# Kernel optimization log

Measured on AMD Instinct MI355X. Metric: run time of the kernel, lower is better.

## Reference

```python
import jax, jax.numpy as jnp
import numpy as np

N = 50000      # nodes
E = 600000     # edges
G = 512        # graphs in batch
F_IN = 128     # input node features
H = 128        # hidden size (both layers)
PH = 128       # pool/classifier hidden size


def setup_inputs() -> dict:
    key = jax.random.key(0)
    ks = jax.random.split(key, 12)
    def lin(k, fi, fo):
        return (jax.random.normal(k, (fi, fo), jnp.float32) / np.sqrt(fi)).astype(jnp.float32)
    return {
        "x": jax.random.normal(ks[0], (N, F_IN), jnp.float32),
        "edge_index": jax.random.randint(ks[1], (2, E), 0, N),
        "batch": jnp.sort(jax.random.randint(ks[2], (N,), 0, G)),
        "W1": lin(ks[3], F_IN, H), "b1": jnp.zeros((H,), jnp.float32),
        "ln1_g": jnp.ones((H,), jnp.float32), "ln1_b": jnp.zeros((H,), jnp.float32),
        "W2": lin(ks[4], H, H), "b2": jnp.zeros((H,), jnp.float32),
        "ln2_g": jnp.ones((H,), jnp.float32), "ln2_b": jnp.zeros((H,), jnp.float32),
        "gate_w1": lin(ks[5], H, PH), "gate_b1": jnp.zeros((PH,), jnp.float32),
        "gate_w2": lin(ks[6], PH, 1), "gate_b2": jnp.zeros((1,), jnp.float32),
        "cls_w1": lin(ks[7], H, PH), "cls_b1": jnp.zeros((PH,), jnp.float32),
        "cls_w2": lin(ks[8], PH, 2), "cls_b2": jnp.zeros((2,), jnp.float32),
    }


def _layer_norm(h, g, b):
    m = h.mean(-1, keepdims=True)
    v = ((h - m) ** 2).mean(-1, keepdims=True)
    return (h - m) * jax.lax.rsqrt(v + 1e-5) * g + b


def _gcn(x, src, dst, norm, W, b):
    # GCNConv: x' = D^{-1/2} (A+I) D^{-1/2} (x W) + b
    h = x @ W
    out = jax.ops.segment_sum(h[src] * norm[:, None], dst, num_segments=N)
    return out + b


def reference(x, edge_index, batch, W1, b1, ln1_g, ln1_b, W2, b2, ln2_g, ln2_b,
              gate_w1, gate_b1, gate_w2, gate_b2, cls_w1, cls_b1, cls_w2, cls_b2):
    loops = jnp.arange(N, dtype=edge_index.dtype)
    src = jnp.concatenate([edge_index[0], loops])
    dst = jnp.concatenate([edge_index[1], loops])
    deg = jax.ops.segment_sum(jnp.ones_like(src, dtype=x.dtype), dst, num_segments=N)
    dinv = jnp.where(deg > 0, jax.lax.rsqrt(jnp.maximum(deg, 1e-12)), 0.0)
    norm = dinv[src] * dinv[dst]  # [(E+N)]

    h = jax.nn.relu(_layer_norm(_gcn(x, src, dst, norm, W1, b1), ln1_g, ln1_b))
    h = jax.nn.relu(_layer_norm(_gcn(h, src, dst, norm, W2, b2), ln2_g, ln2_b))

    # GlobalAttention pooling: gate MLP -> scatter softmax over graphs -> weighted sum
    gate = (jax.nn.relu(h @ gate_w1 + gate_b1) @ gate_w2 + gate_b2)[:, 0]  # [N]
    gmax = jax.ops.segment_max(gate, batch, num_segments=G)
    a = jnp.exp(gate - gmax[batch])
    denom = jax.ops.segment_sum(a, batch, num_segments=G)
    alpha = a / denom[batch]
    pooled = jax.ops.segment_sum(alpha[:, None] * h, batch, num_segments=G)  # [G, H]

    logits = jax.nn.relu(pooled @ cls_w1 + cls_b1) @ cls_w2 + cls_b2  # [G, 2]
    return logits
```

## Files before the change

kernel.cpp:

```cpp
#include <hip/hip_runtime.h>
#include <hip/hip_bf16.h>

typedef short s8v __attribute__((ext_vector_type(8)));
typedef float f4v __attribute__((ext_vector_type(4)));

#define LDA 136

__device__ __forceinline__ unsigned short f2bf(float f) {
  unsigned int u = __builtin_bit_cast(unsigned int, f);
  unsigned int r = u + 0x7fffu + ((u >> 16) & 1u);
  return (unsigned short)(r >> 16);
}
__device__ __forceinline__ float bf2f(unsigned short s) {
  return __builtin_bit_cast(float, ((unsigned int)s) << 16);
}
__device__ __forceinline__ float bflo(unsigned int v) {
  return __builtin_bit_cast(float, (unsigned int)(v << 16));
}
__device__ __forceinline__ float bfhi(unsigned int v) {
  return __builtin_bit_cast(float, (unsigned int)(v & 0xffff0000u));
}
__device__ __forceinline__ unsigned int packbf(float a, float b) {
  return (unsigned int)f2bf(a) | ((unsigned int)f2bf(b) << 16);
}

__device__ __forceinline__ int lower_bound_i(const int* a, int n, int key) {
  int lo = 0, hi = n;
  while (lo < hi) { int mid = (lo + hi) >> 1; if (a[mid] < key) lo = mid + 1; else hi = mid; }
  return lo;
}

__device__ __forceinline__ void gather_node(
    int i, int sub, const int* __restrict__ offs, const int2* __restrict__ col2,
    const float* __restrict__ dinv, const uint4* __restrict__ hu,
    const float* __restrict__ bias, float v[8]) {
  float di = dinv[i];
  float sl = di * di;
  uint4 hv = hu[(size_t)i * 16 + sub];
  float4 b0v = reinterpret_cast<const float4*>(bias)[sub * 2];
  float4 b1v = reinterpret_cast<const float4*>(bias)[sub * 2 + 1];
  v[0] = bflo(hv.x) * sl + b0v.x; v[1] = bfhi(hv.x) * sl + b0v.y;
  v[2] = bflo(hv.y) * sl + b0v.z; v[3] = bfhi(hv.y) * sl + b0v.w;
  v[4] = bflo(hv.z) * sl + b1v.x; v[5] = bfhi(hv.z) * sl + b1v.y;
  v[6] = bflo(hv.w) * sl + b1v.z; v[7] = bfhi(hv.w) * sl + b1v.w;
  int b0 = offs[i], b1 = offs[i + 1];
  int e = b0;
  for (; e + 4 <= b1; e += 4) {
    int2 c0 = col2[e], c1 = col2[e + 1], c2 = col2[e + 2], c3 = col2[e + 3];
    uint4 h0 = hu[(size_t)c0.x * 16 + sub];
    uint4 h1 = hu[(size_t)c1.x * 16 + sub];
    uint4 h2 = hu[(size_t)c2.x * 16 + sub];
    uint4 h3 = hu[(size_t)c3.x * 16 + sub];
    float n0 = __builtin_bit_cast(float, c0.y) * di;
    float n1 = __builtin_bit_cast(float, c1.y) * di;
    float n2 = __builtin_bit_cast(float, c2.y) * di;
    float n3 = __builtin_bit_cast(float, c3.y) * di;
    v[0] += bflo(h0.x) * n0 + bflo(h1.x) * n1 + bflo(h2.x) * n2 + bflo(h3.x) * n3;
    v[1] += bfhi(h0.x) * n0 + bfhi(h1.x) * n1 + bfhi(h2.x) * n2 + bfhi(h3.x) * n3;
    v[2] += bflo(h0.y) * n0 + bflo(h1.y) * n1 + bflo(h2.y) * n2 + bflo(h3.y) * n3;
    v[3] += bfhi(h0.y) * n0 + bfhi(h1.y) * n1 + bfhi(h2.y) * n2 + bfhi(h3.y) * n3;
    v[4] += bflo(h0.z) * n0 + bflo(h1.z) * n1 + bflo(h2.z) * n2 + bflo(h3.z) * n3;
    v[5] += bfhi(h0.z) * n0 + bfhi(h1.z) * n1 + bfhi(h2.z) * n2 + bfhi(h3.z) * n3;
    v[6] += bflo(h0.w) * n0 + bflo(h1.w) * n1 + bflo(h2.w) * n2 + bflo(h3.w) * n3;
    v[7] += bfhi(h0.w) * n0 + bfhi(h1.w) * n1 + bfhi(h2.w) * n2 + bfhi(h3.w) * n3;
  }
  for (; e < b1; ++e) {
    int2 c0 = col2[e];
    uint4 h0 = hu[(size_t)c0.x * 16 + sub];
    float n0 = __builtin_bit_cast(float, c0.y) * di;
    v[0] += bflo(h0.x) * n0; v[1] += bfhi(h0.x) * n0;
    v[2] += bflo(h0.y) * n0; v[3] += bfhi(h0.y) * n0;
    v[4] += bflo(h0.z) * n0; v[5] += bfhi(h0.z) * n0;
    v[6] += bflo(h0.w) * n0; v[7] += bfhi(h0.w) * n0;
  }
}

__device__ __forceinline__ uint4 ln_relu_pack(
    float v[8], int sub, const float* __restrict__ gam, const float* __restrict__ bet) {
  float s = 0.f, q = 0.f;
#pragma unroll
  for (int j = 0; j < 8; ++j) { s += v[j]; q += v[j] * v[j]; }
#pragma unroll
  for (int o = 1; o < 16; o <<= 1) {
    s += __shfl_xor(s, o);
    q += __shfl_xor(q, o);
  }
  float m = s * (1.0f / 128.0f);
  float var = q * (1.0f / 128.0f) - m * m;
  float rs = rsqrtf(var + 1e-5f);
  float4 g0 = reinterpret_cast<const float4*>(gam)[sub * 2];
  float4 g1 = reinterpret_cast<const float4*>(gam)[sub * 2 + 1];
  float4 e0 = reinterpret_cast<const float4*>(bet)[sub * 2];
  float4 e1 = reinterpret_cast<const float4*>(bet)[sub * 2 + 1];
  uint4 ov;
  ov.x = packbf(fmaxf((v[0] - m) * rs * g0.x + e0.x, 0.f), fmaxf((v[1] - m) * rs * g0.y + e0.y, 0.f));
  ov.y = packbf(fmaxf((v[2] - m) * rs * g0.z + e0.z, 0.f), fmaxf((v[3] - m) * rs * g0.w + e0.w, 0.f));
  ov.z = packbf(fmaxf((v[4] - m) * rs * g1.x + e1.x, 0.f), fmaxf((v[5] - m) * rs * g1.y + e1.y, 0.f));
  ov.w = packbf(fmaxf((v[6] - m) * rs * g1.z + e1.z, 0.f), fmaxf((v[7] - m) * rs * g1.w + e1.w, 0.f));
  return ov;
}

__global__ __launch_bounds__(256) void pack_zero(
    const float* __restrict__ Wa, const float* __restrict__ Wb, const float* __restrict__ Wc,
    unsigned short* __restrict__ P, unsigned int* __restrict__ deg, int n) {
  int bid = blockIdx.x;
  if (bid >= 384) {
    int i = (bid - 384) * 256 + threadIdx.x;
    if (i < n) deg[i] = 0u;
    return;
  }
  int gidx = bid * 256 + threadIdx.x;
  int which = gidx >> 15;
  int idx = gidx & 32767;
  const float* W = (which == 0) ? Wa : (which == 1) ? Wb : Wc;
  int j = idx & 15;
  int lane = (idx >> 4) & 63;
  int t = (idx >> 10) & 7;
  int c = (idx >> 13) & 3;
  int k = c * 32 + (lane >> 4) * 8 + (j & 7);
  int nn = t * 16 + (lane & 15);
  float f = W[k * 128 + nn];
  unsigned short hi = f2bf(f);
  unsigned short outv = (j < 8) ? hi : f2bf(f - bf2f(hi));
  P[gidx] = outv;
}

__global__ void accum_deg(const int* __restrict__ dst, unsigned int* __restrict__ deg, int E) {
  int e = blockIdx.x * blockDim.x + threadIdx.x;
  if (e < E) atomicAdd(&deg[dst[e]], 1u);
}

__global__ __launch_bounds__(256) void scanA(const unsigned int* __restrict__ deg,
                                             int* __restrict__ offs, int* __restrict__ partial,
                                             float* __restrict__ dinv, int n) {
  __shared__ int sh[256];
  int t = threadIdx.x;
  int i = blockIdx.x * 256 + t;
  int v = (i < n) ? (int)deg[i] : 0;
  if (i < n) dinv[i] = rsqrtf((float)(deg[i] + 1u));
  sh[t] = v;
  __syncthreads();
  for (int o = 1; o < 256; o <<= 1) {
    int add = (t >= o) ? sh[t - o] : 0;
    __syncthreads();
    sh[t] += add;
    __syncthreads();
  }
  if (i < n) offs[i] = sh[t] - v;
  if (t == 255) partial[blockIdx.x] = sh[255];
}

__global__ __launch_bounds__(256) void scanC(int* __restrict__ offs, const int* __restrict__ partial,
                                             int* __restrict__ cursor, int n, int E) {
  __shared__ int red[256];
  int bid = blockIdx.x;
  int t = threadIdx.x;
  int s = 0;
  for (int j = t; j < bid; j += 256) s += partial[j];
  red[t] = s;
  __syncthreads();
#pragma unroll
  for (int o = 128; o > 0; o >>= 1) {
    if (t < o) red[t] += red[t + o];
    __syncthreads();
  }
  int pre = red[0];
  int i = bid * 256 + t;
  if (i < n) {
    int o = offs[i] + pre;
    offs[i] = o;
    cursor[i] = o;
  }
  if (i == 0) offs[n] = E;
}

__global__ __launch_bounds__(256) void gemm1_scatter(
    const float* __restrict__ in, const unsigned short* __restrict__ P,
    unsigned short* __restrict__ out, int n,
    const int* __restrict__ src, const int* __restrict__ dst,
    int* __restrict__ cursor, int2* __restrict__ col2,
    const float* __restrict__ dinv, int E, int gemmBlocks) {
  if ((int)blockIdx.x >= gemmBlocks) {
    int e = ((int)blockIdx.x - gemmBlocks) * 256 + threadIdx.x;
    if (e < E) {
      int d = dst[e];
      int s = src[e];
      int slot = atomicAdd(&cursor[d], 1);
      col2[slot] = make_int2(s, __builtin_bit_cast(int, dinv[s]));
    }
    return;
  }
  int tid = threadIdx.x;
  int wave = tid >> 6, lane = tid & 63;
  int quad = lane >> 4, col = lane & 15;
  int base = blockIdx.x * 64 + wave * 16;
  int m = base + col;

  f4v acc[8];
#pragma unroll
  for (int t = 0; t < 8; ++t) acc[t] = (f4v){0.f, 0.f, 0.f, 0.f};

  for (int c = 0; c < 4; ++c) {
    s8v ah, al;
    float v[8];
    if (m < n) {
      const float4* xp = reinterpret_cast<const float4*>(in + (size_t)m * 128 + c * 32 + quad * 8);
      float4 v0 = xp[0], v1 = xp[1];
      v[0] = v0.x; v[1] = v0.y; v[2] = v0.z; v[3] = v0.w;
      v[4] = v1.x; v[5] = v1.y; v[6] = v1.z; v[7] = v1.w;
    } else {
#pragma unroll
      for (int j = 0; j < 8; ++j) v[j] = 0.f;
    }
#pragma unroll
    for (int j = 0; j < 8; ++j) {
      unsigned short h = f2bf(v[j]);
      ah[j] = (short)h;
      al[j] = (short)f2bf(v[j] - bf2f(h));
    }
#pragma unroll
    for (int t = 0; t < 8; ++t) {
      const s8v* bp = reinterpret_cast<const s8v*>(&P[((c * 8 + t) * 64 + lane) * 16]);
      s8v bh = bp[0], bl = bp[1];
      acc[t] = __builtin_amdgcn_mfma_f32_16x16x32_bf16(ah, bh, acc[t], 0, 0, 0);
      acc[t] = __builtin_amdgcn_mfma_f32_16x16x32_bf16(ah, bl, acc[t], 0, 0, 0);
      acc[t] = __builtin_amdgcn_mfma_f32_16x16x32_bf16(al, bh, acc[t], 0, 0, 0);
    }
  }
#pragma unroll
  for (int t = 0; t < 8; ++t)
#pragma unroll
    for (int r = 0; r < 4; ++r) {
      int mm = base + quad * 4 + r;
      if (mm < n) out[(size_t)mm * 128 + t * 16 + col] = f2bf(acc[t][r]);
    }
}

__global__ __launch_bounds__(256) void gather_gemm(
    const int* __restrict__ offs, const int2* __restrict__ col2,
    const float* __restrict__ dinv, const unsigned short* __restrict__ h,
    const float* __restrict__ bias, const float* __restrict__ gam,
    const float* __restrict__ bet, const unsigned short* __restrict__ P,
    unsigned short* __restrict__ out, int n) {
  __shared__ unsigned short A[64 * LDA];
  int tid = threadIdx.x;
  int wave = tid >> 6, lane = tid & 63;
  int grp = lane >> 4, sub = lane & 15;
  const uint4* hu = reinterpret_cast<const uint4*>(h);
  int blk = blockIdx.x * 64;
  for (int it = 0; it < 4; ++it) {
    int li = it * 16 + wave * 4 + grp;
    int i = blk + li;
    uint4 ov;
    if (i < n) {
      float v[8];
      gather_node(i, sub, offs, col2, dinv, hu, bias, v);
      ov = ln_relu_pack(v, sub, gam, bet);
    } else {
      ov = make_uint4(0u, 0u, 0u, 0u);
    }
    *reinterpret_cast<uint4*>(&A[li * LDA + sub * 8]) = ov;
  }
  __syncthreads();
  int quad = lane >> 4, col = lane & 15;
  f4v acc[8];
#pragma unroll
  for (int t = 0; t < 8; ++t) acc[t] = (f4v){0.f, 0.f, 0.f, 0.f};
  int liA = wave * 16 + col;
  for (int c = 0; c < 4; ++c) {
    s8v ah = *reinterpret_cast<const s8v*>(&A[liA * LDA + c * 32 + quad * 8]);
#pragma unroll
    for (int t = 0; t < 8; ++t) {
      const s8v* bp = reinterpret_cast<const s8v*>(&P[((c * 8 + t) * 64 + lane) * 16]);
      s8v bh = bp[0], bl = bp[1];
      acc[t] = __builtin_amdgcn_mfma_f32_16x16x32_bf16(ah, bh, acc[t], 0, 0, 0);
      acc[t] = __builtin_amdgcn_mfma_f32_16x16x32_bf16(ah, bl, acc[t], 0, 0, 0);
    }
  }
#pragma unroll
  for (int t = 0; t < 8; ++t)
#pragma unroll
    for (int r = 0; r < 4; ++r) {
      int mm = blk + wave * 16 + quad * 4 + r;
      if (mm < n) out[(size_t)mm * 128 + t * 16 + col] = f2bf(acc[t][r]);
    }
}

__global__ __launch_bounds__(256) void gather_gate(
    const int* __restrict__ offs, const int2* __restrict__ col2,
    const float* __restrict__ dinv, const unsigned short* __restrict__ h,
    const float* __restrict__ bias, const float* __restrict__ gam,
    const float* __restrict__ bet, const unsigned short* __restrict__ P,
    const float* __restrict__ gb1, const float* __restrict__ gw2,
    const float* __restrict__ gb2, unsigned short* __restrict__ hout,
    float* __restrict__ gate, int n) {
  __shared__ unsigned short A[64 * LDA];
  int tid = threadIdx.x;
  int wave = tid >> 6, lane = tid & 63;
  int grp = lane >> 4, sub = lane & 15;
  const uint4* hu = reinterpret_cast<const uint4*>(h);
  int blk = blockIdx.x * 64;
  for (int it = 0; it < 4; ++it) {
    int li = it * 16 + wave * 4 + grp;
    int i = blk + li;
    uint4 ov;
    if (i < n) {
      float v[8];
      gather_node(i, sub, offs, col2, dinv, hu, bias, v);
      ov = ln_relu_pack(v, sub, gam, bet);
      reinterpret_cast<uint4*>(hout)[(size_t)i * 16 + sub] = ov;
    } else {
      ov = make_uint4(0u, 0u, 0u, 0u);
    }
    *reinterpret_cast<uint4*>(&A[li * LDA + sub * 8]) = ov;
  }
  __syncthreads();
  int quad = lane >> 4, col = lane & 15;
  f4v acc[8];
#pragma unroll
  for (int t = 0; t < 8; ++t) acc[t] = (f4v){0.f, 0.f, 0.f, 0.f};
  int liA = wave * 16 + col;
  for (int c = 0; c < 4; ++c) {
    s8v ah = *reinterpret_cast<const s8v*>(&A[liA * LDA + c * 32 + quad * 8]);
#pragma unroll
    for (int t = 0; t < 8; ++t) {
      const s8v* bp = reinterpret_cast<const s8v*>(&P[((c * 8 + t) * 64 + lane) * 16]);
      s8v bh = bp[0], bl = bp[1];
      acc[t] = __builtin_amdgcn_mfma_f32_16x16x32_bf16(ah, bh, acc[t], 0, 0, 0);
      acc[t] = __builtin_amdgcn_mfma_f32_16x16x32_bf16(ah, bl, acc[t], 0, 0, 0);
    }
  }
  float bv[8], g2[8];
#pragma unroll
  for (int t = 0; t < 8; ++t) {
    bv[t] = gb1[t * 16 + col];
    g2[t] = gw2[t * 16 + col];
  }
  float gb2v = gb2[0];
#pragma unroll
  for (int r = 0; r < 4; ++r) {
    float p = 0.f;
#pragma unroll
    for (int t = 0; t < 8; ++t)
      p += fmaxf(acc[t][r] + bv[t], 0.f) * g2[t];
#pragma unroll
    for (int o = 1; o < 16; o <<= 1) p += __shfl_xor(p, o);
    int mm = blk + wave * 16 + quad * 4 + r;
    if (col == 0 && mm < n) gate[mm] = p + gb2v;
  }
}

__global__ __launch_bounds__(256) void pool_cls(
    float* __restrict__ gate, const unsigned short* __restrict__ h,
    const int* __restrict__ batch,
    const float* __restrict__ w1, const float* __restrict__ b1,
    const float* __restrict__ w2, const float* __restrict__ b2,
    float* __restrict__ out, int n) {
  int g = blockIdx.x;
  int tid = threadIdx.x;
  __shared__ float red[256];
  __shared__ float red2[256];
  __shared__ float p[128];
  __shared__ float r[128];
  int lo = lower_bound_i(batch, n, g);
  int hi = lower_bound_i(batch, n, g + 1);
  if (lo >= hi) {
    if (tid < 128) p[tid] = 0.0f;
  } else {
    float m = -3.0e38f;
    for (int i = lo + tid; i < hi; i += 256) m = fmaxf(m, gate[i]);
    red[tid] = m;
    __syncthreads();
#pragma unroll
    for (int o = 128; o > 0; o >>= 1) {
      if (tid < o) red[tid] = fmaxf(red[tid], red[tid + o]);
      __syncthreads();
    }
    m = red[0];
    __syncthreads();
    float s = 0.0f;
    for (int i = lo + tid; i < hi; i += 256) {
      float e = __expf(gate[i] - m);
      gate[i] = e;
      s += e;
    }
    red[tid] = s;
    __syncthreads();
#pragma unroll
    for (int o = 128; o > 0; o >>= 1) {
      if (tid < o) red[tid] += red[tid + o];
      __syncthreads();
    }
    float inv = 1.0f / red[0];
    __syncthreads();
    const unsigned int* hu = reinterpret_cast<const unsigned int*>(h);
    int j = tid & 63, rgp = tid >> 6;
    float a0 = 0.f, a1 = 0.f;
    int i = lo + rgp;
    for (; i + 4 < hi; i += 8) {
      unsigned int p0 = hu[(size_t)i * 64 + j];
      unsigned int p1 = hu[(size_t)(i + 4) * 64 + j];
      float w0 = gate[i], w1v = gate[i + 4];
      a0 += bflo(p0) * w0 + bflo(p1) * w1v;
      a1 += bfhi(p0) * w0 + bfhi(p1) * w1v;
    }
    if (i < hi) {
      unsigned int p0 = hu[(size_t)i * 64 + j];
      float w0 = gate[i];
      a0 += bflo(p0) * w0;
      a1 += bfhi(p0) * w0;
    }
    red[tid] = a0;
    red2[tid] = a1;
    __syncthreads();
    if (tid < 64) {
      p[2 * tid]     = (red[tid] + red[tid + 64] + red[tid + 128] + red[tid + 192]) * inv;
      p[2 * tid + 1] = (red2[tid] + red2[tid + 64] + red2[tid + 128] + red2[tid + 192]) * inv;
    }
  }
  __syncthreads();
  int j = tid & 127, half = tid >> 7;
  float acc = 0.0f;
#pragma unroll 8
  for (int k = half * 64; k < half * 64 + 64; ++k)
    acc = fmaf(p[k], w1[k * 128 + j], acc);
  red[tid] = acc;
  __syncthreads();
  if (tid < 128) r[tid] = fmaxf(red[tid] + red[tid + 128] + b1[tid], 0.0f);
  __syncthreads();
  if (tid < 2) {
    float a = 0.0f;
    for (int k = 0; k < 128; ++k) a = fmaf(r[k], w2[k * 2 + tid], a);
    out[g * 2 + tid] = a + b2[tid];
  }
}

static inline size_t alup(size_t x) { return (x + 255) & ~(size_t)255; }

extern "C" void kernel_launch(void* const* d_in, const int* in_sizes, int n_in,
                              void* d_out, int out_size, void* d_ws, size_t ws_size,
                              hipStream_t stream) {
  const float* x    = (const float*)d_in[0];
  const int*   ei   = (const int*)d_in[1];
  const int*   bat  = (const int*)d_in[2];
  const float* W1   = (const float*)d_in[3];
  const float* b1   = (const float*)d_in[4];
  const float* ln1g = (const float*)d_in[5];
  const float* ln1b = (const float*)d_in[6];
  const float* W2   = (const float*)d_in[7];
  const float* b2   = (const float*)d_in[8];
  const float* ln2g = (const float*)d_in[9];
  const float* ln2b = (const float*)d_in[10];
  const float* gw1  = (const float*)d_in[11];
  const float* gb1  = (const float*)d_in[12];
  const float* gw2  = (const float*)d_in[13];
  const float* gb2  = (const float*)d_in[14];
  const float* cw1  = (const float*)d_in[15];
  const float* cb1  = (const float*)d_in[16];
  const float* cw2  = (const float*)d_in[17];
  const float* cb2  = (const float*)d_in[18];

  const int N = in_sizes[2];
  const int E = in_sizes[1] / 2;
  const int G = out_size / 2;
  const int* src = ei;
  const int* dst = ei + E;

  int nb256 = (N + 255) / 256;
  int eb256 = (E + 255) / 256;
  int mfmaB = (N + 63) / 64;

  char* base = (char*)d_ws;
  unsigned int* deg = (unsigned int*)base; base += alup((size_t)N * 4);
  float* dinv = (float*)base;              base += alup((size_t)N * 4);
  int* offs = (int*)base;                  base += alup((size_t)(N + 1) * 4);
  int* cursor = (int*)base;                base += alup((size_t)N * 4);
  int* partial = (int*)base;               base += alup((size_t)nb256 * 4);
  int2* col2 = (int2*)base;                base += alup((size_t)E * 8);
  unsigned short* pW = (unsigned short*)base; base += alup((size_t)3 * 32768 * 2);
  unsigned short* hbuf = (unsigned short*)base;  base += alup((size_t)N * 128 * 2);
  unsigned short* hbuf2 = (unsigned short*)base; base += alup((size_t)N * 128 * 2);
  unsigned short* hout = (unsigned short*)base;  base += alup((size_t)N * 128 * 2);
  float* gate = (float*)base;              base += alup((size_t)N * 4);

  unsigned short* pW1 = pW;
  unsigned short* pW2 = pW + 32768;
  unsigned short* pG1 = pW + 65536;

  float* out = (float*)d_out;

  pack_zero<<<384 + nb256, 256, 0, stream>>>(W1, W2, gw1, pW, deg, N);
  accum_deg<<<eb256, 256, 0, stream>>>(dst, deg, E);
  scanA<<<nb256, 256, 0, stream>>>(deg, offs, partial, dinv, N);
  scanC<<<nb256, 256, 0, stream>>>(offs, partial, cursor, N, E);
  gemm1_scatter<<<mfmaB + eb256, 256, 0, stream>>>(x, pW1, hbuf, N,
                                                   src, dst, cursor, col2, dinv, E, mfmaB);
  gather_gemm<<<mfmaB, 256, 0, stream>>>(offs, col2, dinv, hbuf, b1, ln1g, ln1b,
                                         pW2, hbuf2, N);
  gather_gate<<<mfmaB, 256, 0, stream>>>(offs, col2, dinv, hbuf2, b2, ln2g, ln2b,
                                         pG1, gb1, gw2, gb2, hout, gate, N);
  pool_cls<<<G, 256, 0, stream>>>(gate, hout, bat, cw1, cb1, cw2, cb2, out, N);
}
```

Baseline: 266.0 us.

## Fold source-side degree normalization into GEMM epilogue and shrink CSR to indices

The GEMM epilogues now pre-scale each output row by dinv of that node, so the gather only sums neighbor rows and multiplies once by the destination dinv. This lets the CSR array hold plain int source indices instead of (index, dinv) pairs, halving edge-array traffic and removing the per-edge dinv load during scatter and the per-edge multiplies in the gather. It adds a rounding step, because the pre-scaled values are stored in bf16.

After: 272.3 us. +2.4%, slower.

```diff
diff --git a/kernel.cpp b/kernel.cpp
--- a/kernel.cpp
+++ b/kernel.cpp
@@ -30,48 +30,38 @@
   return lo;
 }
 
-__device__ __forceinline__ void gather_node(
-    int i, int sub, const int* __restrict__ offs, const int2* __restrict__ col2,
-    const float* __restrict__ dinv, const uint4* __restrict__ hu,
-    const float* __restrict__ bias, float v[8]) {
-  float di = dinv[i];
-  float sl = di * di;
+__device__ __forceinline__ void gather_sum(
+    int i, int sub, const int* __restrict__ offs, const int* __restrict__ col,
+    const uint4* __restrict__ hu, float acc[8]) {
   uint4 hv = hu[(size_t)i * 16 + sub];
-  float4 b0v = reinterpret_cast<const float4*>(bias)[sub * 2];
-  float4 b1v = reinterpret_cast<const float4*>(bias)[sub * 2 + 1];
-  v[0] = bflo(hv.x) * sl + b0v.x; v[1] = bfhi(hv.x) * sl + b0v.y;
-  v[2] = bflo(hv.y) * sl + b0v.z; v[3] = bfhi(hv.y) * sl + b0v.w;
-  v[4] = bflo(hv.z) * sl + b1v.x; v[5] = bfhi(hv.z) * sl + b1v.y;
-  v[6] = bflo(hv.w) * sl + b1v.z; v[7] = bfhi(hv.w) * sl + b1v.w;
+  acc[0] = bflo(hv.x); acc[1] = bfhi(hv.x);
+  acc[2] = bflo(hv.y); acc[3] = bfhi(hv.y);
+  acc[4] = bflo(hv.z); acc[5] = bfhi(hv.z);
+  acc[6] = bflo(hv.w); acc[7] = bfhi(hv.w);
   int b0 = offs[i], b1 = offs[i + 1];
   int e = b0;
   for (; e + 4 <= b1; e += 4) {
-    int2 c0 = col2[e], c1 = col2[e + 1], c2 = col2[e + 2], c3 = col2[e + 3];
-    uint4 h0 = hu[(size_t)c0.x * 16 + sub];
-    uint4 h1 = hu[(size_t)c1.x * 16 + sub];
-    uint4 h2 = hu[(size_t)c2.x * 16 + sub];
-    uint4 h3 = hu[(size_t)c3.x * 16 + sub];
-    float n0 = __builtin_bit_cast(float, c0.y) * di;
-    float n1 = __builtin_bit_cast(float, c1.y) * di;
-    float n2 = __builtin_bit_cast(float, c2.y) * di;
-    float n3 = __builtin_bit_cast(float, c3.y) * di;
-    v[0] += bflo(h0.x) * n0 + bflo(h1.x) * n1 + bflo(h2.x) * n2 + bflo(h3.x) * n3;
-    v[1] += bfhi(h0.x) * n0 + bfhi(h1.x) * n1 + bfhi(h2.x) * n2 + bfhi(h3.x) * n3;
-    v[2] += bflo(h0.y) * n0 + bflo(h1.y) * n1 + bflo(h2.y) * n2 + bflo(h3.y) * n3;
-    v[3] += bfhi(h0.y) * n0 + bfhi(h1.y) * n1 + bfhi(h2.y) * n2 + bfhi(h3.y) * n3;
-    v[4] += bflo(h0.z) * n0 + bflo(h1.z) * n1 + bflo(h2.z) * n2 + bflo(h3.z) * n3;
-    v[5] += bfhi(h0.z) * n0 + bfhi(h1.z) * n1 + bfhi(h2.z) * n2 + bfhi(h3.z) * n3;
-    v[6] += bflo(h0.w) * n0 + bflo(h1.w) * n1 + bflo(h2.w) * n2 + bflo(h3.w) * n3;
-    v[7] += bfhi(h0.w) * n0 + bfhi(h1.w) * n1 + bfhi(h2.w) * n2 + bfhi(h3.w) * n3;
+    int s0 = col[e], s1 = col[e + 1], s2 = col[e + 2], s3 = col[e + 3];
+    uint4 h0 = hu[(size_t)s0 * 16 + sub];
+    uint4 h1 = hu[(size_t)s1 * 16 + sub];
+    uint4 h2 = hu[(size_t)s2 * 16 + sub];
+    uint4 h3 = hu[(size_t)s3 * 16 + sub];
+    acc[0] += bflo(h0.x) + bflo(h1.x) + bflo(h2.x) + bflo(h3.x);
+    acc[1] += bfhi(h0.x) + bfhi(h1.x) + bfhi(h2.x) + bfhi(h3.x);
+    acc[2] += bflo(h0.y) + bflo(h1.y) + bflo(h2.y) + bflo(h3.y);
+    acc[3] += bfhi(h0.y) + bfhi(h1.y) + bfhi(h2.y) + bfhi(h3.y);
+    acc[4] += bflo(h0.z) + bflo(h1.z) + bflo(h2.z) + bflo(h3.z);
+    acc[5] += bfhi(h0.z) + bfhi(h1.z) + bfhi(h2.z) + bfhi(h3.z);
+    acc[6] += bflo(h0.w) + bflo(h1.w) + bflo(h2.w) + bflo(h3.w);
+    acc[7] += bfhi(h0.w) + bfhi(h1.w) + bfhi(h2.w) + bfhi(h3.w);
   }
   for (; e < b1; ++e) {
-    int2 c0 = col2[e];
-    uint4 h0 = hu[(size_t)c0.x * 16 + sub];
-    float n0 = __builtin_bit_cast(float, c0.y) * di;
-    v[0] += bflo(h0.x) * n0; v[1] += bfhi(h0.x) * n0;
-    v[2] += bflo(h0.y) * n0; v[3] += bfhi(h0.y) * n0;
-    v[4] += bflo(h0.z) * n0; v[5] += bfhi(h0.z) * n0;
-    v[6] += bflo(h0.w) * n0; v[7] += bfhi(h0.w) * n0;
+    int s0 = col[e];
+    uint4 h0 = hu[(size_t)s0 * 16 + sub];
+    acc[0] += bflo(h0.x); acc[1] += bfhi(h0.x);
+    acc[2] += bflo(h0.y); acc[3] += bfhi(h0.y);
+    acc[4] += bflo(h0.z); acc[5] += bfhi(h0.z);
+    acc[6] += bflo(h0.w); acc[7] += bfhi(h0.w);
   }
 }
 
@@ -98,6 +88,16 @@
   ov.z = packbf(fmaxf((v[4] - m) * rs * g1.x + e1.x, 0.f), fmaxf((v[5] - m) * rs * g1.y + e1.y, 0.f));
   ov.w = packbf(fmaxf((v[6] - m) * rs * g1.z + e1.z, 0.f), fmaxf((v[7] - m) * rs * g1.w + e1.w, 0.f));
   return ov;
+}
+
+__device__ __forceinline__ void scale_bias(
+    float acc[8], float di, int sub, const float* __restrict__ bias, float v[8]) {
+  float4 b0v = reinterpret_cast<const float4*>(bias)[sub * 2];
+  float4 b1v = reinterpret_cast<const float4*>(bias)[sub * 2 + 1];
+  v[0] = acc[0] * di + b0v.x; v[1] = acc[1] * di + b0v.y;
+  v[2] = acc[2] * di + b0v.z; v[3] = acc[3] * di + b0v.w;
+  v[4] = acc[4] * di + b1v.x; v[5] = acc[5] * di + b1v.y;
+  v[6] = acc[6] * di + b1v.z; v[7] = acc[7] * di + b1v.w;
 }
 
 __global__ __launch_bounds__(256) void pack_zero(
@@ -178,23 +178,22 @@
     const float* __restrict__ in, const unsigned short* __restrict__ P,
     unsigned short* __restrict__ out, int n,
     const int* __restrict__ src, const int* __restrict__ dst,
-    int* __restrict__ cursor, int2* __restrict__ col2,
+    int* __restrict__ cursor, int* __restrict__ col,
     const float* __restrict__ dinv, int E, int gemmBlocks) {
   if ((int)blockIdx.x >= gemmBlocks) {
     int e = ((int)blockIdx.x - gemmBlocks) * 256 + threadIdx.x;
     if (e < E) {
       int d = dst[e];
-      int s = src[e];
       int slot = atomicAdd(&cursor[d], 1);
-      col2[slot] = make_int2(s, __builtin_bit_cast(int, dinv[s]));
+      col[slot] = src[e];
     }
     return;
   }
   int tid = threadIdx.x;
   int wave = tid >> 6, lane = tid & 63;
-  int quad = lane >> 4, col = lane & 15;
+  int quad = lane >> 4, c16 = lane & 15;
   int base = blockIdx.x * 64 + wave * 16;
-  int m = base + col;
+  int m = base + c16;
 
   f4v acc[8];
 #pragma unroll
@@ -227,17 +226,23 @@
       acc[t] = __builtin_amdgcn_mfma_f32_16x16x32_bf16(al, bh, acc[t], 0, 0, 0);
     }
   }
+  float dv[4];
+#pragma unroll
+  for (int r = 0; r < 4; ++r) {
+    int mm = base + quad * 4 + r;
+    dv[r] = (mm < n) ? dinv[mm] : 0.f;
+  }
 #pragma unroll
   for (int t = 0; t < 8; ++t)
 #pragma unroll
     for (int r = 0; r < 4; ++r) {
       int mm = base + quad * 4 + r;
-      if (mm < n) out[(size_t)mm * 128 + t * 16 + col] = f2bf(acc[t][r]);
+      if (mm < n) out[(size_t)mm * 128 + t * 16 + c16] = f2bf(acc[t][r] * dv[r]);
     }
 }
 
 __global__ __launch_bounds__(256) void gather_gemm(
-    const int* __restrict__ offs, const int2* __restrict__ col2,
+    const int* __restrict__ offs, const int* __restrict__ col,
     const float* __restrict__ dinv, const unsigned short* __restrict__ h,
     const float* __restrict__ bias, const float* __restrict__ gam,
     const float* __restrict__ bet, const unsigned short* __restrict__ P,
@@ -253,8 +258,9 @@
     int i = blk + li;
     uint4 ov;
     if (i < n) {
-      float v[8];
-      gather_node(i, sub, offs, col2, dinv, hu, bias, v);
+      float acc[8], v[8];
+      gather_sum(i, sub, offs, col, hu, acc);
+      scale_bias(acc, dinv[i], sub, bias, v);
       ov = ln_relu_pack(v, sub, gam, bet);
     } else {
       ov = make_uint4(0u, 0u, 0u, 0u);
@@ -262,11 +268,11 @@
     *reinterpret_cast<uint4*>(&A[li * LDA + sub * 8]) = ov;
   }
   __syncthreads();
-  int quad = lane >> 4, col = lane & 15;
+  int quad = lane >> 4, c16 = lane & 15;
   f4v acc[8];
 #pragma unroll
   for (int t = 0; t < 8; ++t) acc[t] = (f4v){0.f, 0.f, 0.f, 0.f};
-  int liA = wave * 16 + col;
+  int liA = wave * 16 + c16;
   for (int c = 0; c < 4; ++c) {
     s8v ah = *reinterpret_cast<const s8v*>(&A[liA * LDA + c * 32 + quad * 8]);
 #pragma unroll
@@ -277,17 +283,23 @@
       acc[t] = __builtin_amdgcn_mfma_f32_16x16x32_bf16(ah, bl, acc[t], 0, 0, 0);
     }
   }
+  float dv[4];
+#pragma unroll
+  for (int r = 0; r < 4; ++r) {
+    int mm = blk + wave * 16 + quad * 4 + r;
+    dv[r] = (mm < n) ? dinv[mm] : 0.f;
+  }
 #pragma unroll
   for (int t = 0; t < 8; ++t)
 #pragma unroll
     for (int r = 0; r < 4; ++r) {
       int mm = blk + wave * 16 + quad * 4 + r;
-      if (mm < n) out[(size_t)mm * 128 + t * 16 + col] = f2bf(acc[t][r]);
+      if (mm < n) out[(size_t)mm * 128 + t * 16 + c16] = f2bf(acc[t][r] * dv[r]);
     }
 }
 
 __global__ __launch_bounds__(256) void gather_gate(
-    const int* __restrict__ offs, const int2* __restrict__ col2,
+    const int* __restrict__ offs, const int* __restrict__ col,
     const float* __restrict__ dinv, const unsigned short* __restrict__ h,
     const float* __restrict__ bias, const float* __restrict__ gam,
     const float* __restrict__ bet, const unsigned short* __restrict__ P,
@@ -305,8 +317,9 @@
     int i = blk + li;
     uint4 ov;
     if (i < n) {
-      float v[8];
-      gather_node(i, sub, offs, col2, dinv, hu, bias, v);
+      float acc[8], v[8];
+      gather_sum(i, sub, offs, col, hu, acc);
+      scale_bias(acc, dinv[i], sub, bias, v);
       ov = ln_relu_pack(v, sub, gam, bet);
       reinterpret_cast<uint4*>(hout)[(size_t)i * 16 + sub] = ov;
     } else {
@@ -315,11 +328,11 @@
     *reinterpret_cast<uint4*>(&A[li * LDA + sub * 8]) = ov;
   }
   __syncthreads();
-  int quad = lane >> 4, col = lane & 15;
+  int quad = lane >> 4, c16 = lane & 15;
   f4v acc[8];
 #pragma unroll
   for (int t = 0; t < 8; ++t) acc[t] = (f4v){0.f, 0.f, 0.f, 0.f};
-  int liA = wave * 16 + col;
+  int liA = wave * 16 + c16;
   for (int c = 0; c < 4; ++c) {
     s8v ah = *reinterpret_cast<const s8v*>(&A[liA * LDA + c * 32 + quad * 8]);
 #pragma unroll
@@ -333,8 +346,8 @@
   float bv[8], g2[8];
 #pragma unroll
   for (int t = 0; t < 8; ++t) {
-    bv[t] = gb1[t * 16 + col];
-    g2[t] = gw2[t * 16 + col];
+    bv[t] = gb1[t * 16 + c16];
+    g2[t] = gw2[t * 16 + c16];
   }
   float gb2v = gb2[0];
 #pragma unroll
@@ -346,7 +359,7 @@
 #pragma unroll
     for (int o = 1; o < 16; o <<= 1) p += __shfl_xor(p, o);
     int mm = blk + wave * 16 + quad * 4 + r;
-    if (col == 0 && mm < n) gate[mm] = p + gb2v;
+    if (c16 == 0 && mm < n) gate[mm] = p + gb2v;
   }
 }
 
@@ -476,7 +489,7 @@
   int* offs = (int*)base;                  base += alup((size_t)(N + 1) * 4);
   int* cursor = (int*)base;                base += alup((size_t)N * 4);
   int* partial = (int*)base;               base += alup((size_t)nb256 * 4);
-  int2* col2 = (int2*)base;                base += alup((size_t)E * 8);
+  int* col = (int*)base;                   base += alup((size_t)E * 4);
   unsigned short* pW = (unsigned short*)base; base += alup((size_t)3 * 32768 * 2);
   unsigned short* hbuf = (unsigned short*)base;  base += alup((size_t)N * 128 * 2);
   unsigned short* hbuf2 = (unsigned short*)base; base += alup((size_t)N * 128 * 2);
@@ -494,10 +507,10 @@
   scanA<<<nb256, 256, 0, stream>>>(deg, offs, partial, dinv, N);
   scanC<<<nb256, 256, 0, stream>>>(offs, partial, cursor, N, E);
   gemm1_scatter<<<mfmaB + eb256, 256, 0, stream>>>(x, pW1, hbuf, N,
-                                                   src, dst, cursor, col2, dinv, E, mfmaB);
-  gather_gemm<<<mfmaB, 256, 0, stream>>>(offs, col2, dinv, hbuf, b1, ln1g, ln1b,
+                                                   src, dst, cursor, col, dinv, E, mfmaB);
+  gather_gemm<<<mfmaB, 256, 0, stream>>>(offs, col, dinv, hbuf, b1, ln1g, ln1b,
                                          pW2, hbuf2, N);
-  gather_gate<<<mfmaB, 256, 0, stream>>>(offs, col2, dinv, hbuf2, b2, ln2g, ln2b,
+  gather_gate<<<mfmaB, 256, 0, stream>>>(offs, col, dinv, hbuf2, b2, ln2g, ln2b,
                                          pG1, gb1, gw2, gb2, hout, gate, N);
   pool_cls<<<G, 256, 0, stream>>>(gate, hout, bat, cw1, cb1, cw2, cb2, out, N);
 }
```
